# Optimization experiments

Measured on AMD Instinct MI355X. Metric: run time of the kernel, lower is better.

## Reference

```python
import jax, jax.numpy as jnp
from jax import lax
import numpy as np

B, C, H, W, K = 8, 256, 128, 128, 4


def setup_inputs() -> dict:
    key = jax.random.key(0)
    ks = jax.random.split(key, 21)
    s = 0.05
    return {
        'frm_feat': jax.random.normal(ks[0], (B, C, H, W), jnp.float32),
        'other_feat': jax.random.normal(ks[1], (B, C, H, W), jnp.float32),
        'conv3x3_w': jax.random.normal(ks[2], (C, 2 * C, 3, 3), jnp.float32) * (1.0 / np.sqrt(2 * C * 9).astype(np.float32)),
        'conv3x3_b': jax.random.normal(ks[3], (C,), jnp.float32) * s,
        'a1_w': jax.random.normal(ks[4], (C, 2), jnp.float32) * s,
        'a1_b': jax.random.normal(ks[5], (C,), jnp.float32) * s,
        'a2_w': jax.random.normal(ks[6], (C, 2), jnp.float32) * s,
        'a2_b': jax.random.normal(ks[7], (C,), jnp.float32) * s,
        'a3_w': jax.random.normal(ks[8], (C, 2), jnp.float32) * s,
        'a3_b': jax.random.normal(ks[9], (C,), jnp.float32) * s,
        'ug_w': jax.random.normal(ks[10], (K, C), jnp.float32) * (1.0 / np.sqrt(C).astype(np.float32)),
        'ug_b': jax.random.normal(ks[11], (K,), jnp.float32) * s,
        'recon_w': jax.random.normal(ks[12], (C, C), jnp.float32) * (1.0 / np.sqrt(C).astype(np.float32)),
        'recon_b': jax.random.normal(ks[13], (C,), jnp.float32) * s,
        'sp_w': jax.random.normal(ks[14], (), jnp.float32),
        'sp_b': jax.random.normal(ks[15], (), jnp.float32) * s,
        'spa_w': jax.random.normal(ks[16], (C, C), jnp.float32) * (1.0 / np.sqrt(C).astype(np.float32)),
        'spa_b': jax.random.normal(ks[17], (C,), jnp.float32) * s,
        'spm_w': jax.random.normal(ks[18], (C, C), jnp.float32) * (1.0 / np.sqrt(C).astype(np.float32)),
        'spm_b': jax.random.normal(ks[19], (C,), jnp.float32) * s,
        'alpha': jnp.float32(0.5),
    }


def _make_U(mode, aw, ab, ug_w, ug_b):
    # mode: [B, N, M] -> U: [B, N, K] (softmax over rank K)
    avg = jnp.mean(mode, axis=2)           # [B, N]
    mx = jnp.max(mode, axis=2)             # [B, N]
    feat = jnp.stack([avg, mx], axis=1)    # [B, 2, N]
    feat = jnp.einsum('co,bon->bcn', aw, feat) + ab[None, :, None]  # adapter 1x1 conv: [B, C, N]
    logits = jnp.einsum('kc,bcn->bnk', ug_w, feat) + ug_b           # U_gen 1x1 conv: [B, N, K]
    return jax.nn.softmax(logits, axis=-1)


def reference(frm_feat, other_feat, conv3x3_w, conv3x3_b, a1_w, a1_b, a2_w, a2_b,
              a3_w, a3_b, ug_w, ug_b, recon_w, recon_b, sp_w, sp_b,
              spa_w, spa_b, spm_w, spm_b, alpha):
    b, c, h, w = frm_feat.shape
    x = jnp.concatenate([frm_feat, other_feat], axis=1)  # [B, 2C, H, W]
    Fm = lax.conv_general_dilated(x, conv3x3_w, (1, 1), 'SAME',
                                  dimension_numbers=('NCHW', 'OIHW', 'NCHW'))
    Fm = Fm + conv3x3_b[None, :, None, None]
    Fm = jnp.where(Fm >= 0, Fm, 0.01 * Fm)  # LeakyReLU(0.01)

    # Three mode unfoldings (same math as torch permute/reshape chains)
    mode1 = Fm.reshape(b, c, h * w)                     # [B, C, HW]
    mode2 = jnp.transpose(Fm, (0, 3, 1, 2)).reshape(b, w, c * h)  # [B, W, CH]
    mode3 = jnp.transpose(Fm, (0, 2, 1, 3)).reshape(b, h, c * w)  # [B, H, CW]

    U1 = _make_U(mode1, a1_w, a1_b, ug_w, ug_b)  # [B, C, K]
    U2 = _make_U(mode2, a2_w, a2_b, ug_w, ug_b)  # [B, W, K]
    U3 = _make_U(mode3, a3_w, a3_b, ug_w, ug_b)  # [B, H, K]

    # CP outer-product reconstruction summed over rank, already in [B,C,H,W] layout
    cp = jnp.einsum('bck,bwk,bhk->bchw', U1, U2, U3)
    cp = jnp.einsum('oc,bchw->bohw', recon_w, cp) + recon_b[None, :, None, None]

    # spatial attention: sigmoid(1x1 conv on U3 @ U2^T)
    spatial_att = jax.nn.sigmoid(sp_w * jnp.einsum('bhk,bwk->bhw', U3, U2)[:, None] + sp_b)  # [B,1,H,W]

    # spectral attention
    U23 = jnp.concatenate([U2, U3], axis=1)              # [B, W+H, K]
    F_spe = jnp.einsum('bck,bnk->bcn', U1, U23)          # [B, C, W+H]
    g_avg = jnp.mean(F_spe, axis=-1)                     # [B, C]
    g_max = jnp.max(F_spe, axis=-1)                      # [B, C]
    spec = jax.nn.sigmoid(g_avg @ spa_w.T + spa_b + g_max @ spm_w.T + spm_b)
    spec = jax.nn.sigmoid(spec)[:, :, None, None]        # double sigmoid as in source, [B,C,1,1]

    Watt = spec * spatial_att                            # [B, C, H, W]
    fused = alpha * Watt * frm_feat + (1.0 - alpha) * (1.0 - Watt) * other_feat
    return fused, cp
```

## Files before the change

### kernel.cpp

```cpp
#include <hip/hip_runtime.h>
#include <math.h>

#define BB 8
#define CC 256
#define HH 128
#define WW 128
#define CP_OFF 33554432

#define ZB_OFF   0
#define P1S_OFF  256
#define P1M_OFF  262400
#define P2S_OFF  524544
#define P2M_OFF  525568
#define P3S_OFF  526592
#define P3M_OFF  527616
#define U2_OFF   528640
#define U3_OFF   532736
#define V1_OFF   536832
#define SPEC_OFF 545024
#define WS_ZERO_BYTES (528640 * 4)

typedef __attribute__((ext_vector_type(8))) short bf16x8;
typedef __attribute__((ext_vector_type(4))) float f32x4;

static __device__ __forceinline__ unsigned short f2bf(float f) {
    unsigned u = __float_as_uint(f);
    unsigned r = u + 0x7FFFu + ((u >> 16) & 1u);
    return (unsigned short)(r >> 16);
}
static __device__ __forceinline__ unsigned fkey(float f) {
    unsigned u = __float_as_uint(f);
    return (u & 0x80000000u) ? ~u : (u | 0x80000000u);
}
static __device__ __forceinline__ float fkeydec(unsigned k) {
    return __uint_as_float((k & 0x80000000u) ? (k & 0x7FFFFFFFu) : ~k);
}
static __device__ __forceinline__ void gl_lds16(const void* g, void* l) {
    typedef const __attribute__((address_space(1))) unsigned int* gas_t;
    typedef __attribute__((address_space(3))) unsigned int* las_t;
    gas_t gp = (gas_t)(uintptr_t)g;
    las_t lp = (las_t)(unsigned int)(uintptr_t)l;
    __builtin_amdgcn_global_load_lds(gp, lp, 16, 0, 0);
}

__global__ __launch_bounds__(256) void wt_kernel(
    const float* __restrict__ cw, unsigned short* __restrict__ Wt)
{
    const int g = blockIdx.x * 256 + threadIdx.x;
    const int co = g >> 9, ci = g & 511;
    const float* s = cw + (size_t)g * 9;
    #pragma unroll
    for (int t = 0; t < 9; t++)
        Wt[((size_t)t * 256 + co) * 512 + ci] = f2bf(s[t]);
}

__global__ __launch_bounds__(256) void xt_kernel(
    const float* __restrict__ frm, const float* __restrict__ oth,
    unsigned short* __restrict__ Xt)
{
    const int w = threadIdx.x & 127, half = threadIdx.x >> 7;
    const int h = blockIdx.x, b = blockIdx.y;
    const float* src = half ? oth : frm;
    const size_t inbase = (((size_t)b * 256) << 14) + ((size_t)h << 7) + w;
    unsigned short* op = Xt + ((((size_t)(b * 128 + h) * 128) + w) << 9) + half * 256;
    #pragma unroll 2
    for (int c8 = 0; c8 < 32; c8++) {
        unsigned short u[8];
        #pragma unroll
        for (int j = 0; j < 8; j++)
            u[j] = f2bf(src[inbase + (((size_t)(c8 * 8 + j)) << 14)]);
        uint4 pk;
        pk.x = (unsigned)u[0] | ((unsigned)u[1] << 16);
        pk.y = (unsigned)u[2] | ((unsigned)u[3] << 16);
        pk.z = (unsigned)u[4] | ((unsigned)u[5] << 16);
        pk.w = (unsigned)u[6] | ((unsigned)u[7] << 16);
        *(uint4*)(op + c8 * 8) = pk;
    }
}

__global__ __launch_bounds__(256, 2) void conv_mfma(
    const unsigned short* __restrict__ Wt,
    const unsigned short* __restrict__ Xt,
    const float* __restrict__ cb,
    const unsigned short* __restrict__ zb,
    float* __restrict__ p1s, unsigned* __restrict__ p1m,
    float* __restrict__ p2s, unsigned* __restrict__ p2m,
    float* __restrict__ p3s, unsigned* __restrict__ p3m)
{
    __shared__ __align__(16) unsigned short lA[2][1536 * 8];
    __shared__ __align__(16) unsigned short lB[2][544 * 8];

    const int tid = threadIdx.x;
    const int swz = (blockIdx.x & 7) * 256 + (blockIdx.x >> 3);
    const int b = swz >> 8;
    const int h = (swz >> 1) & 127;
    const int cohalf = swz & 1;

    const int lane = tid & 63, wid = tid >> 6;
    const int wm = wid & 1, wn = wid >> 1;
    const int l15 = lane & 15, l4 = lane >> 4;

    f32x4 acc[4][4];
    #pragma unroll
    for (int m = 0; m < 4; m++)
        #pragma unroll
        for (int n = 0; n < 4; n++)
            acc[m][n] = (f32x4){0.f, 0.f, 0.f, 0.f};

    auto stage = [&](int q, int bufi) {
        const int kh = q >> 4;
        const int ci0 = (q & 15) << 5;
        const int hr = h + kh - 1;
        const bool hv = (hr >= 0) && (hr < HH);
        const size_t xrow = ((size_t)(b * 128 + (hv ? hr : 0))) << 16;
        unsigned short* A = lA[bufi];
        unsigned short* Bl = lB[bufi];
        #pragma unroll
        for (int it = 0; it < 6; it++) {
            const int slot = it * 256 + tid;
            const int kw = slot >> 9;
            const int unit = slot & 511;
            const int ku = unit >> 7, co = unit & 127;
            const unsigned short* g = Wt +
                ((size_t)((kh * 3 + kw) * 256 + cohalf * 128 + co) * 512 + ci0 + ku * 8);
            gl_lds16(g, &A[slot * 8]);
        }
        #pragma unroll
        for (int it = 0; it < 3; it++) {
            const int slot = it * 256 + tid;
            if (slot < 544) {
                const int ku = slot / 136;
                const int wi = slot - ku * 136;
                const int wg = wi - 1;
                const bool v = hv && (wg >= 0) && (wg < WW);
                const unsigned short* g = v
                    ? Xt + (xrow + (((size_t)wg) << 9) + ci0 + ku * 8)
                    : zb;
                gl_lds16(g, &Bl[slot * 8]);
            }
        }
    };

    stage(0, 0);
    __syncthreads();

    #pragma unroll 1
    for (int q = 0; q < 48; q++) {
        const int cur = q & 1;
        if (q < 47) stage(q + 1, cur ^ 1);

        const unsigned short* A = lA[cur];
        const unsigned short* Bl = lB[cur];
        __builtin_amdgcn_s_setprio(1);
        #pragma unroll
        for (int kw = 0; kw < 3; kw++) {
            bf16x8 af[4], bfr[4];
            #pragma unroll
            for (int m = 0; m < 4; m++) {
                const int unit = kw * 512 + l4 * 128 + wm * 64 + m * 16 + l15;
                af[m] = *(const bf16x8*)&A[unit * 8];
            }
            #pragma unroll
            for (int n = 0; n < 4; n++) {
                const int unit = l4 * 136 + wn * 64 + n * 16 + l15 + kw;
                bfr[n] = *(const bf16x8*)&Bl[unit * 8];
            }
            #pragma unroll
            for (int m = 0; m < 4; m++)
                #pragma unroll
                for (int n = 0; n < 4; n++)
                    acc[m][n] = __builtin_amdgcn_mfma_f32_16x16x32_bf16(
                        af[m], bfr[n], acc[m][n], 0, 0, 0);
        }
        __builtin_amdgcn_s_setprio(0);
        __syncthreads();
    }

    const int cob = cohalf * 128 + wm * 64;
    float t1s[4][4], t1m[4][4], s2[4], x2[4];
    #pragma unroll
    for (int n = 0; n < 4; n++) { s2[n] = 0.f; x2[n] = -INFINITY; }

    #pragma unroll
    for (int m = 0; m < 4; m++) {
        const float4 bb4 = *(const float4*)&cb[cob + m * 16 + l4 * 4];
        float bbv[4] = { bb4.x, bb4.y, bb4.z, bb4.w };
        #pragma unroll
        for (int r = 0; r < 4; r++) { t1s[m][r] = 0.f; t1m[m][r] = -INFINITY; }
        #pragma unroll
        for (int n = 0; n < 4; n++) {
            #pragma unroll
            for (int r = 0; r < 4; r++) {
                float v = acc[m][n][r] + bbv[r];
                v = (v >= 0.f) ? v : 0.01f * v;
                t1s[m][r] += v;
                t1m[m][r] = fmaxf(t1m[m][r], v);
                s2[n] += v;
                x2[n] = fmaxf(x2[n], v);
            }
        }
    }
    #pragma unroll
    for (int m = 0; m < 4; m++)
        #pragma unroll
        for (int r = 0; r < 4; r++) {
            float s = t1s[m][r], x = t1m[m][r];
            #pragma unroll
            for (int off = 1; off <= 8; off <<= 1) {
                s += __shfl_xor(s, off);
                x = fmaxf(x, __shfl_xor(x, off));
            }
            t1s[m][r] = s; t1m[m][r] = x;
        }
    if (l15 == 0) {
        #pragma unroll
        for (int m = 0; m < 4; m++)
            #pragma unroll
            for (int r = 0; r < 4; r++) {
                const int co = cob + m * 16 + l4 * 4 + r;
                const int idx = (b * 256 + co) * 128 + h;
                atomicAdd(&p1s[idx], t1s[m][r]);
                atomicMax(&p1m[idx], fkey(t1m[m][r]));
            }
    }
    float s3 = 0.f, x3 = -INFINITY;
    #pragma unroll
    for (int n = 0; n < 4; n++) {
        float s = s2[n], x = x2[n];
        s += __shfl_xor(s, 16); s += __shfl_xor(s, 32);
        x = fmaxf(x, __shfl_xor(x, 16)); x = fmaxf(x, __shfl_xor(x, 32));
        if (l4 == n) {
            const int w = wn * 64 + n * 16 + l15;
            atomicAdd(&p2s[b * 128 + w], s);
            atomicMax(&p2m[b * 128 + w], fkey(x));
        }
        s3 += s; x3 = fmaxf(x3, x);
    }
    #pragma unroll
    for (int off = 1; off <= 8; off <<= 1) {
        s3 += __shfl_xor(s3, off);
        x3 = fmaxf(x3, __shfl_xor(x3, off));
    }
    if (lane == 0) {
        atomicAdd(&p3s[b * 128 + h], s3);
        atomicMax(&p3m[b * 128 + h], fkey(x3));
    }
}

__device__ inline float blockSum256(float v, float* red)
{
    #pragma unroll
    for (int off = 32; off >= 1; off >>= 1) v += __shfl_xor(v, off);
    const int wave = threadIdx.x >> 6, lane = threadIdx.x & 63;
    __syncthreads();
    if (lane == 0) red[wave] = v;
    __syncthreads();
    return red[0] + red[1] + red[2] + red[3];
}

__device__ inline void softmax4(const float* A, const float* M, const float* Bc,
                                float avg, float mx, float* u)
{
    float l0 = fmaf(A[0], avg, fmaf(M[0], mx, Bc[0]));
    float l1 = fmaf(A[1], avg, fmaf(M[1], mx, Bc[1]));
    float l2 = fmaf(A[2], avg, fmaf(M[2], mx, Bc[2]));
    float l3 = fmaf(A[3], avg, fmaf(M[3], mx, Bc[3]));
    const float mm = fmaxf(fmaxf(l0, l1), fmaxf(l2, l3));
    const float e0 = expf(l0 - mm), e1 = expf(l1 - mm);
    const float e2 = expf(l2 - mm), e3 = expf(l3 - mm);
    const float inv = 1.f / (e0 + e1 + e2 + e3);
    u[0] = e0 * inv; u[1] = e1 * inv; u[2] = e2 * inv; u[3] = e3 * inv;
}

__global__ void make_u_kernel(
    const float* __restrict__ p1s, const unsigned* __restrict__ p1m,
    const float* __restrict__ p2s, const unsigned* __restrict__ p2m,
    const float* __restrict__ p3s, const unsigned* __restrict__ p3m,
    const float* __restrict__ a1w, const float* __restrict__ a1b,
    const float* __restrict__ a2w, const float* __restrict__ a2b,
    const float* __restrict__ a3w, const float* __restrict__ a3b,
    const float* __restrict__ ugw, const float* __restrict__ ugb,
    const float* __restrict__ rw,
    const float* __restrict__ spaw, const float* __restrict__ spab,
    const float* __restrict__ spmw, const float* __restrict__ spmb,
    float* __restrict__ U2g, float* __restrict__ U3g,
    float* __restrict__ V1g, float* __restrict__ specg)
{
    const int b = blockIdx.x, tid = threadIdx.x;

    __shared__ float red[4];
    __shared__ float coefA[3][4], coefM[3][4], coefB[3][4];
    __shared__ float U1s[256][4], U2s[128][4], U3s[128][4];
    __shared__ float gavg[256], gmax[256];

    const float* aws[3]  = { a1w, a2w, a3w };
    const float* abs_[3] = { a1b, a2b, a3b };
    for (int m = 0; m < 3; m++) {
        for (int k = 0; k < 4; k++) {
            const float u = ugw[k * 256 + tid];
            float va = u * aws[m][tid * 2 + 0];
            float vm = u * aws[m][tid * 2 + 1];
            float vb = u * abs_[m][tid];
            va = blockSum256(va, red);
            vm = blockSum256(vm, red);
            vb = blockSum256(vb, red);
            if (tid == 0) {
                coefA[m][k] = va; coefM[m][k] = vm; coefB[m][k] = vb + ugb[k];
            }
        }
    }
    __syncthreads();

    {
        const float* ps = p1s + ((size_t)b * 256 + tid) * 128;
        const unsigned* pm = p1m + ((size_t)b * 256 + tid) * 128;
        float s = 0.f, mx = -INFINITY;
        for (int hh = 0; hh < 128; hh++) {
            s += ps[hh];
            mx = fmaxf(mx, fkeydec(pm[hh]));
        }
        float u[4];
        softmax4(coefA[0], coefM[0], coefB[0], s * (1.f / 16384.f), mx, u);
        U1s[tid][0] = u[0]; U1s[tid][1] = u[1]; U1s[tid][2] = u[2]; U1s[tid][3] = u[3];
    }
    if (tid < 128) {
        const float avg = p2s[b * 128 + tid] * (1.f / 32768.f);
        const float mx  = fkeydec(p2m[b * 128 + tid]);
        float u[4];
        softmax4(coefA[1], coefM[1], coefB[1], avg, mx, u);
        float* g = U2g + ((size_t)b * 128 + tid) * 4;
        for (int k = 0; k < 4; k++) { U2s[tid][k] = u[k]; g[k] = u[k]; }
    } else {
        const int hh = tid - 128;
        const float avg = p3s[b * 128 + hh] * (1.f / 32768.f);
        const float mx  = fkeydec(p3m[b * 128 + hh]);
        float u[4];
        softmax4(coefA[2], coefM[2], coefB[2], avg, mx, u);
        float* g = U3g + ((size_t)b * 128 + hh) * 4;
        for (int k = 0; k < 4; k++) { U3s[hh][k] = u[k]; g[k] = u[k]; }
    }
    __syncthreads();

    {
        float v0 = 0.f, v1 = 0.f, v2 = 0.f, v3 = 0.f;
        const float* rrow = rw + (size_t)tid * 256;
        for (int c2 = 0; c2 < 256; c2++) {
            const float r = rrow[c2];
            v0 = fmaf(r, U1s[c2][0], v0);
            v1 = fmaf(r, U1s[c2][1], v1);
            v2 = fmaf(r, U1s[c2][2], v2);
            v3 = fmaf(r, U1s[c2][3], v3);
        }
        float* vp = V1g + ((size_t)b * 256 + tid) * 4;
        vp[0] = v0; vp[1] = v1; vp[2] = v2; vp[3] = v3;
    }
    {
        const float a0 = U1s[tid][0], a1 = U1s[tid][1];
        const float a2 = U1s[tid][2], a3 = U1s[tid][3];
        float s = 0.f, m = -INFINITY;
        for (int n = 0; n < 256; n++) {
            const float* u23 = (n < 128) ? U2s[n] : U3s[n - 128];
            const float val = a0 * u23[0] + a1 * u23[1] + a2 * u23[2] + a3 * u23[3];
            s += val; m = fmaxf(m, val);
        }
        gavg[tid] = s * (1.f / 256.f);
        gmax[tid] = m;
    }
    __syncthreads();
    {
        float s = spab[tid] + spmb[tid];
        const float* wa = spaw + (size_t)tid * 256;
        const float* wmp = spmw + (size_t)tid * 256;
        for (int c2 = 0; c2 < 256; c2++) {
            s = fmaf(gavg[c2], wa[c2], s);
            s = fmaf(gmax[c2], wmp[c2], s);
        }
        float sg = 1.f / (1.f + expf(-s));
        sg = 1.f / (1.f + expf(-sg));
        specg[b * 256 + tid] = sg;
    }
}

__global__ __launch_bounds__(256) void final_kernel(
    const float* __restrict__ frm, const float* __restrict__ oth,
    const float* __restrict__ U2g, const float* __restrict__ U3g,
    const float* __restrict__ V1g, const float* __restrict__ specg,
    const float* __restrict__ rb,  const float* __restrict__ spw,
    const float* __restrict__ spb, const float* __restrict__ alphap,
    float* __restrict__ out)
{
    const int w  = threadIdx.x & 127;
    const int cc = threadIdx.x >> 7;
    const int h  = blockIdx.x;
    const int c  = blockIdx.y * 2 + cc;
    const int b  = blockIdx.z;

    const float4 u2 = *(const float4*)(U2g + ((size_t)b * 128 + w) * 4);
    const float4 u3 = *(const float4*)(U3g + ((size_t)b * 128 + h) * 4);
    const float4 v1 = *(const float4*)(V1g + ((size_t)b * 256 + c) * 4);

    const float p0 = u2.x * u3.x, p1 = u2.y * u3.y;
    const float p2 = u2.z * u3.z, p3 = u2.w * u3.w;
    const float dot = p0 + p1 + p2 + p3;
    const float att = 1.f / (1.f + expf(-(spw[0] * dot + spb[0])));
    const float cp  = v1.x * p0 + v1.y * p1 + v1.z * p2 + v1.w * p3 + rb[c];

    const float spec  = specg[b * 256 + c];
    const float Watt  = spec * att;
    const float alpha = alphap[0];

    const size_t idx = (((size_t)b * 256 + c) << 14) + ((size_t)h << 7) + w;
    const float f = frm[idx], o = oth[idx];
    out[idx]          = alpha * Watt * f + (1.f - alpha) * (1.f - Watt) * o;
    out[CP_OFF + idx] = cp;
}

extern "C" void kernel_launch(void* const* d_in, const int* in_sizes, int n_in,
                              void* d_out, int out_size, void* d_ws, size_t ws_size,
                              hipStream_t stream)
{
    const float* frm   = (const float*)d_in[0];
    const float* oth   = (const float*)d_in[1];
    const float* cw    = (const float*)d_in[2];
    const float* cb    = (const float*)d_in[3];
    const float* a1w   = (const float*)d_in[4];
    const float* a1b   = (const float*)d_in[5];
    const float* a2w   = (const float*)d_in[6];
    const float* a2b   = (const float*)d_in[7];
    const float* a3w   = (const float*)d_in[8];
    const float* a3b   = (const float*)d_in[9];
    const float* ugw   = (const float*)d_in[10];
    const float* ugb   = (const float*)d_in[11];
    const float* rw    = (const float*)d_in[12];
    const float* rb    = (const float*)d_in[13];
    const float* spw   = (const float*)d_in[14];
    const float* spb   = (const float*)d_in[15];
    const float* spaw  = (const float*)d_in[16];
    const float* spab  = (const float*)d_in[17];
    const float* spmw  = (const float*)d_in[18];
    const float* spmb  = (const float*)d_in[19];
    const float* alpha = (const float*)d_in[20];

    float* out = (float*)d_out;
    float* ws  = (float*)d_ws;

    unsigned short* Wt = (unsigned short*)out;
    unsigned short* Xt = (unsigned short*)(out + CP_OFF);

    float*    zb  = ws + ZB_OFF;
    float*    p1s = ws + P1S_OFF;
    unsigned* p1m = (unsigned*)(ws + P1M_OFF);
    float*    p2s = ws + P2S_OFF;
    unsigned* p2m = (unsigned*)(ws + P2M_OFF);
    float*    p3s = ws + P3S_OFF;
    unsigned* p3m = (unsigned*)(ws + P3M_OFF);
    float*    U2g = ws + U2_OFF;
    float*    U3g = ws + U3_OFF;
    float*    V1g = ws + V1_OFF;
    float*    spc = ws + SPEC_OFF;

    hipMemsetAsync(d_ws, 0, WS_ZERO_BYTES, stream);

    wt_kernel<<<dim3(512), 256, 0, stream>>>(cw, Wt);
    xt_kernel<<<dim3(HH, BB), 256, 0, stream>>>(frm, oth, Xt);

    conv_mfma<<<dim3(2048), 256, 0, stream>>>(
        Wt, Xt, cb, (const unsigned short*)zb,
        p1s, p1m, p2s, p2m, p3s, p3m);

    make_u_kernel<<<dim3(BB), 256, 0, stream>>>(
        p1s, p1m, p2s, p2m, p3s, p3m,
        a1w, a1b, a2w, a2b, a3w, a3b, ugw, ugb,
        rw, spaw, spab, spmw, spmb,
        U2g, U3g, V1g, spc);

    final_kernel<<<dim3(HH, CC / 2, BB), 256, 0, stream>>>(
        frm, oth, U2g, U3g, V1g, spc, rb, spw, spb, alpha, out);
}
```

Measured before the change: 1.120 ms.

## Precompute conv staging addresses, pad LDS rows, and overlap loads with partial vmcnt waits

The conv MFMA kernel now computes per-thread global source pointers and LDS destinations once, outside the K loop, so each stage step only adds a scalar offset. LDS rows are padded (130/138 units instead of 128/136) to cut bank conflicts on fragment reads. The double-buffer loop replaces __syncthreads with explicit barriers and s_waitcnt vmcnt(9), so the next tile's async loads stay in flight while the current tile is computed. The hand-tuned wait count depends on exact instruction counts and is fragile if the compiler reorders or adds memory ops.

After: 1.141 ms. No clear change (+1.9%).

```diff
diff --git a/kernel.cpp b/kernel.cpp
--- a/kernel.cpp
+++ b/kernel.cpp
@@ -87,8 +87,8 @@
     float* __restrict__ p2s, unsigned* __restrict__ p2m,
     float* __restrict__ p3s, unsigned* __restrict__ p3m)
 {
-    __shared__ __align__(16) unsigned short lA[2][1536 * 8];
-    __shared__ __align__(16) unsigned short lB[2][544 * 8];
+    __shared__ __align__(16) unsigned short lA[2][1560 * 8];
+    __shared__ __align__(16) unsigned short lB[2][552 * 8];
 
     const int tid = threadIdx.x;
     const int swz = (blockIdx.x & 7) * 256 + (blockIdx.x >> 3);
@@ -100,6 +100,30 @@
     const int wm = wid & 1, wn = wid >> 1;
     const int l15 = lane & 15, l4 = lane >> 4;
 
+    const unsigned short* baseA[6];
+    int dstA[6];
+    #pragma unroll
+    for (int i = 0; i < 6; i++) {
+        const int ch = i * 4 + wid;
+        const int r = ch >> 1, half = ch & 1;
+        const int kw = r >> 2, ku = r & 3;
+        baseA[i] = Wt + (size_t)(cohalf * 128 + half * 64 + lane) * 512
+                      + kw * 131072 + ku * 8;
+        dstA[i] = (r * 130 + half * 64) * 8;
+    }
+    const unsigned short* baseB[3];
+    bool okB[3];
+    int dstB[3];
+    #pragma unroll
+    for (int j = 0; j < 3; j++) {
+        const int wi = j * 64 + lane;
+        const int wg = wi - 1;
+        okB[j] = (wg >= 0) && (wg < WW);
+        baseB[j] = Xt + (size_t)b * 8388608
+                      + (size_t)(okB[j] ? wg : 0) * 512 + wid * 8;
+        dstB[j] = (wid * 138 + j * 64) * 8;
+    }
+
     f32x4 acc[4][4];
     #pragma unroll
     for (int m = 0; m < 4; m++)
@@ -112,57 +136,36 @@
         const int ci0 = (q & 15) << 5;
         const int hr = h + kh - 1;
         const bool hv = (hr >= 0) && (hr < HH);
-        const size_t xrow = ((size_t)(b * 128 + (hv ? hr : 0))) << 16;
-        unsigned short* A = lA[bufi];
-        unsigned short* Bl = lB[bufi];
-        #pragma unroll
-        for (int it = 0; it < 6; it++) {
-            const int slot = it * 256 + tid;
-            const int kw = slot >> 9;
-            const int unit = slot & 511;
-            const int ku = unit >> 7, co = unit & 127;
-            const unsigned short* g = Wt +
-                ((size_t)((kh * 3 + kw) * 256 + cohalf * 128 + co) * 512 + ci0 + ku * 8);
-            gl_lds16(g, &A[slot * 8]);
-        }
-        #pragma unroll
-        for (int it = 0; it < 3; it++) {
-            const int slot = it * 256 + tid;
-            if (slot < 544) {
-                const int ku = slot / 136;
-                const int wi = slot - ku * 136;
-                const int wg = wi - 1;
-                const bool v = hv && (wg >= 0) && (wg < WW);
-                const unsigned short* g = v
-                    ? Xt + (xrow + (((size_t)wg) << 9) + ci0 + ku * 8)
-                    : zb;
-                gl_lds16(g, &Bl[slot * 8]);
-            }
+        const int aoff = kh * 393216 + ci0;
+        const int boff = (hv ? hr : 0) * 65536 + ci0;
+        #pragma unroll
+        for (int i = 0; i < 6; i++)
+            gl_lds16(baseA[i] + aoff, &lA[bufi][dstA[i]]);
+        #pragma unroll
+        for (int j = 0; j < 2; j++) {
+            const unsigned short* s = (hv && okB[j]) ? (baseB[j] + boff) : zb;
+            gl_lds16(s, &lB[bufi][dstB[j]]);
+        }
+        {
+            const unsigned short* s = (hv && okB[2]) ? (baseB[2] + boff) : zb;
+            if (lane < 8) gl_lds16(s, &lB[bufi][dstB[2]]);
         }
     };
 
-    stage(0, 0);
-    __syncthreads();
-
-    #pragma unroll 1
-    for (int q = 0; q < 48; q++) {
-        const int cur = q & 1;
-        if (q < 47) stage(q + 1, cur ^ 1);
-
-        const unsigned short* A = lA[cur];
+    auto compute = [&](int cur) {
+        const unsigned short* A  = lA[cur];
         const unsigned short* Bl = lB[cur];
-        __builtin_amdgcn_s_setprio(1);
         #pragma unroll
         for (int kw = 0; kw < 3; kw++) {
             bf16x8 af[4], bfr[4];
             #pragma unroll
             for (int m = 0; m < 4; m++) {
-                const int unit = kw * 512 + l4 * 128 + wm * 64 + m * 16 + l15;
+                const int unit = (kw * 4 + l4) * 130 + wm * 64 + m * 16 + l15;
                 af[m] = *(const bf16x8*)&A[unit * 8];
             }
             #pragma unroll
             for (int n = 0; n < 4; n++) {
-                const int unit = l4 * 136 + wn * 64 + n * 16 + l15 + kw;
+                const int unit = l4 * 138 + wn * 64 + n * 16 + l15 + kw;
                 bfr[n] = *(const bf16x8*)&Bl[unit * 8];
             }
             #pragma unroll
@@ -172,9 +175,29 @@
                     acc[m][n] = __builtin_amdgcn_mfma_f32_16x16x32_bf16(
                         af[m], bfr[n], acc[m][n], 0, 0, 0);
         }
+    };
+
+    stage(0, 0);
+
+    #pragma unroll 1
+    for (int q = 0; q < 47; q++) {
+        const int cur = q & 1;
+        stage(q + 1, cur ^ 1);
+        asm volatile("s_waitcnt vmcnt(9)" ::: "memory");
+        __builtin_amdgcn_s_barrier();
+        __builtin_amdgcn_sched_barrier(0);
+        __builtin_amdgcn_s_setprio(1);
+        compute(cur);
         __builtin_amdgcn_s_setprio(0);
-        __syncthreads();
-    }
+        __builtin_amdgcn_sched_barrier(0);
+        __builtin_amdgcn_s_barrier();
+    }
+    asm volatile("s_waitcnt vmcnt(0)" ::: "memory");
+    __builtin_amdgcn_s_barrier();
+    __builtin_amdgcn_sched_barrier(0);
+    __builtin_amdgcn_s_setprio(1);
+    compute(1);
+    __builtin_amdgcn_s_setprio(0);
 
     const int cob = cohalf * 128 + wm * 64;
     float t1s[4][4], t1m[4][4], s2[4], x2[4];
```
